# Optimization experiments

Hardware: AMD Instinct MI355X
Metric: run time of the kernel (lower is better)

The kernel has to match this reference:

```python
import jax, jax.numpy as jnp
import numpy as np

B, C, H, W = 8, 48, 192, 192
N = H * W


def _bn_train(x, gamma, beta, eps=1e-5):
    # BatchNorm2d in training mode: biased batch stats over (B, H, W) per channel
    mean = jnp.mean(x, axis=(0, 2, 3), keepdims=True)
    var = jnp.var(x, axis=(0, 2, 3), keepdims=True)
    xn = (x - mean) * jax.lax.rsqrt(var + eps)
    return xn * gamma[None, :, None, None] + beta[None, :, None, None]


def _conv(x, w, b, pad):
    y = jax.lax.conv_general_dilated(
        x, w, window_strides=(1, 1), padding=[(pad, pad), (pad, pad)],
        dimension_numbers=('NCHW', 'OIHW', 'NCHW'))
    return y + b[None, :, None, None]


def setup_inputs() -> dict:
    key = jax.random.key(0)
    ks = jax.random.split(key, 16)
    s = 0.05
    inp = {
        'input_feature': jax.random.normal(ks[0], (B, C, H, W), jnp.float32),
        'fb': jax.random.normal(ks[1], (B, C, H, W), jnp.float32),
        'fc': jax.random.normal(ks[2], (B, C, H, W), jnp.float32),
        'fd': jax.random.normal(ks[3], (B, C, H, W), jnp.float32),
        'Wa': jax.random.normal(ks[4], (C, C), jnp.float32) * s,
        'Wb': jax.random.normal(ks[5], (C, C), jnp.float32) * s,
        'Wc': jax.random.normal(ks[6], (C, C), jnp.float32) * s,
        'Wd': jax.random.normal(ks[7], (C, C), jnp.float32) * s,
        'fuse_w': jax.random.normal(ks[8], (C, 4 * C, 1, 1), jnp.float32) * s,
        'fuse_b': jnp.zeros((C,), jnp.float32),
        'fuse_gamma': jnp.ones((C,), jnp.float32),
        'fuse_beta': jnp.zeros((C,), jnp.float32),
        'gamma_cam': jnp.full((1,), 0.5, jnp.float32),  # nn.Parameter (init 0; nonzero for testing)
        'out_w': jax.random.normal(ks[9], (C, C, 3, 3), jnp.float32) * s,
        'out_b': jnp.zeros((C,), jnp.float32),
        'out_gamma': jnp.ones((C,), jnp.float32),
        'out_beta': jnp.zeros((C,), jnp.float32),
    }
    return inp


def reference(input_feature, fb, fc, fd, Wa, Wb, Wc, Wd,
              fuse_w, fuse_b, fuse_gamma, fuse_beta, gamma_cam,
              out_w, out_b, out_gamma, out_beta):
    b, c, h, w = input_feature.shape
    n = h * w
    # Linear over channel dim: x.view(B,C,N).permute -> [B,N,C] @ W.T -> permute back = [B,C,N]
    def lin(x, Wm):
        return jnp.einsum('oc,bcn->bon', Wm, x.reshape(b, c, n))

    q = lin(input_feature, Wa)                      # [B,C,N] shared query
    K = jnp.stack([q, lin(fb, Wb), lin(fc, Wc), lin(fd, Wd)], axis=0)  # [4,B,C,N] (k==v)

    # Fused 4-branch channel attention: energy [4,B,C,C]
    energy = jnp.einsum('bcn,sbdn->sbcd', q, K)
    energy_new = jnp.max(energy, axis=-1, keepdims=True) - energy  # reversed softmax logits
    attention = jax.nn.softmax(energy_new, axis=-1)
    out4 = jnp.einsum('sbcd,sbdn->sbcn', attention, K)              # [4,B,C,N]

    # concat along channel dim in branch order -> [B,4C,H,W]
    cat = out4.transpose(1, 0, 2, 3).reshape(b, 4 * c, h, w)

    atten = jax.nn.relu(_bn_train(_conv(cat, fuse_w, fuse_b, pad=0), fuse_gamma, fuse_beta))
    out = gamma_cam[0] * atten + input_feature
    out = jax.nn.relu(_bn_train(_conv(out, out_w, out_b, pad=1), out_gamma, out_beta))
    return out
```

## Files before the change

### kernel.cpp

```cpp
#include <hip/hip_runtime.h>
#include <hip/hip_bf16.h>

#define C 48
#define C4 192
#define HW 192
#define NPIX (HW * HW)
#define BATCH 8
#define CNT (BATCH * NPIX)

#define APRE_OFF   0ull
#define G_OFF      14155776ull
#define STATS_OFF  14229504ull
#define M2_OFF     14229696ull
#define MIDT_BYTE  57213696ull
#define WB_BYTE    85525248ull

typedef __attribute__((ext_vector_type(8))) short short8;
typedef __attribute__((ext_vector_type(4))) float f32x4;

static __device__ __forceinline__ unsigned pkbf(float a, float b) {
    union { __hip_bfloat162 h; unsigned u; } t;
    t.h = __float22bfloat162_rn(make_float2(a, b));
    return t.u;
}
static __device__ __forceinline__ float lo2f(unsigned p) { return __uint_as_float(p << 16); }
static __device__ __forceinline__ float hi2f(unsigned p) { return __uint_as_float(p & 0xffff0000u); }
static __device__ __forceinline__ short f2bfs(float f) { return (short)(pkbf(f, f) & 0xffffu); }

__global__ __launch_bounds__(256, 3) void k_gram_mfma(
    const float* __restrict__ x0, const float* __restrict__ x1,
    const float* __restrict__ x2, const float* __restrict__ x3,
    float* __restrict__ G)
{
    __shared__ short hibuf[C4 * 68];
    __shared__ short lobuf[C4 * 68];
    int b = blockIdx.y;
    int n0 = blockIdx.x * 256;
    int tid = threadIdx.x;
    int wid = tid >> 6, lane = tid & 63, col = lane & 15, quad = lane >> 4;

    const float* x0b = x0 + (size_t)b * C * NPIX;
    const float* x1b = x1 + (size_t)b * C * NPIX;
    const float* x2b = x2 + (size_t)b * C * NPIX;
    const float* x3b = x3 + (size_t)b * C * NPIX;

    f32x4 acc[3][3];
#pragma unroll
    for (int mt = 0; mt < 3; ++mt)
#pragma unroll
        for (int nt = 0; nt < 3; ++nt)
            acc[mt][nt] = (f32x4){0.f, 0.f, 0.f, 0.f};

    int scr = tid >> 4;
    int n4 = (tid & 15) * 4;

#define GRAM_LOAD(dst, nb)                                                      \
    _Pragma("unroll")                                                           \
    for (int it = 0; it < 12; ++it) {                                           \
        const float* xb = (it / 3 == 0) ? x0b : (it / 3 == 1) ? x1b             \
                        : (it / 3 == 2) ? x2b : x3b;                            \
        dst[it] = *(const float4*)(xb + (size_t)(scr + (it % 3) * 16) * NPIX    \
                                      + (nb) + n4);                             \
    }

#define GRAM_PACK(src)                                                          \
    _Pragma("unroll")                                                           \
    for (int it = 0; it < 12; ++it) {                                           \
        int ch = scr + it * 16;                                                 \
        float4 v = src[it];                                                     \
        unsigned h01 = pkbf(v.x, v.y), h23 = pkbf(v.z, v.w);                    \
        float r0 = v.x - lo2f(h01), r1 = v.y - hi2f(h01);                       \
        float r2 = v.z - lo2f(h23), r3 = v.w - hi2f(h23);                       \
        unsigned l01 = pkbf(r0, r1), l23 = pkbf(r2, r3);                        \
        *(uint2*)&hibuf[ch * 68 + n4] = make_uint2(h01, h23);                   \
        *(uint2*)&lobuf[ch * 68 + n4] = make_uint2(l01, l23);                   \
    }

#define GRAM_MMA()                                                              \
    _Pragma("unroll")                                                           \
    for (int kb = 0; kb < 2; ++kb) {                                            \
        int ko = kb * 32 + quad * 8;                                            \
        short8 ah[3], al[3], bh[3], bl[3];                                      \
        _Pragma("unroll")                                                       \
        for (int mt = 0; mt < 3; ++mt) {                                        \
            ah[mt] = *(const short8*)&hibuf[(mt * 16 + col) * 68 + ko];         \
            al[mt] = *(const short8*)&lobuf[(mt * 16 + col) * 68 + ko];         \
        }                                                                       \
        _Pragma("unroll")                                                       \
        for (int nt = 0; nt < 3; ++nt) {                                        \
            int row = (wid * 3 + nt) * 16 + col;                                \
            bh[nt] = *(const short8*)&hibuf[row * 68 + ko];                     \
            bl[nt] = *(const short8*)&lobuf[row * 68 + ko];                     \
        }                                                                       \
        _Pragma("unroll")                                                       \
        for (int mt = 0; mt < 3; ++mt)                                          \
            _Pragma("unroll")                                                   \
            for (int nt = 0; nt < 3; ++nt) {                                    \
                acc[mt][nt] = __builtin_amdgcn_mfma_f32_16x16x32_bf16(          \
                    ah[mt], bh[nt], acc[mt][nt], 0, 0, 0);                      \
                acc[mt][nt] = __builtin_amdgcn_mfma_f32_16x16x32_bf16(          \
                    ah[mt], bl[nt], acc[mt][nt], 0, 0, 0);                      \
                acc[mt][nt] = __builtin_amdgcn_mfma_f32_16x16x32_bf16(          \
                    al[mt], bh[nt], acc[mt][nt], 0, 0, 0);                      \
            }                                                                   \
    }

    float4 preA[12], preB[12];
    GRAM_LOAD(preA, n0)
    GRAM_LOAD(preB, n0 + 64)

#pragma unroll
    for (int sp = 0; sp < 2; ++sp) {
        GRAM_PACK(preA)
        __syncthreads();
        if (sp < 1) { GRAM_LOAD(preA, n0 + (2 * sp + 2) * 64) }
        GRAM_MMA()
        __syncthreads();
        GRAM_PACK(preB)
        __syncthreads();
        if (sp < 1) { GRAM_LOAD(preB, n0 + (2 * sp + 3) * 64) }
        GRAM_MMA()
        __syncthreads();
    }
#undef GRAM_LOAD
#undef GRAM_PACK
#undef GRAM_MMA

#pragma unroll
    for (int mt = 0; mt < 3; ++mt)
#pragma unroll
        for (int nt = 0; nt < 3; ++nt) {
            int g = (wid * 3 + nt) * 16 + col;
            int s = g / C, d = g - s * C;
#pragma unroll
            for (int j = 0; j < 4; ++j) {
                int c = mt * 16 + quad * 4 + j;
                atomicAdd(&G[(((size_t)s * BATCH + b) * C + c) * C + d],
                          acc[mt][nt][j]);
            }
        }
}

__global__ __launch_bounds__(256) void k_small(
    const float* __restrict__ G,
    const float* __restrict__ Wa, const float* __restrict__ Wb,
    const float* __restrict__ Wc, const float* __restrict__ Wd,
    const float* __restrict__ fuse_w, float* __restrict__ M2g)
{
    int s = blockIdx.x, b = blockIdx.y;
    const float* Ws = (s == 0) ? Wa : (s == 1) ? Wb : (s == 2) ? Wc : Wd;

    __shared__ float g[C * C], wsm[C * C], wam[C * C], fw[C * C];
    __shared__ float t[C * C], e[C * C], m[C * C];
    int tid = threadIdx.x;

    const float* Gb = G + ((size_t)s * BATCH + b) * C * C;
    for (int k = tid; k < C * C; k += 256) {
        g[k] = Gb[k];
        wsm[k] = Ws[k];
        wam[k] = Wa[k];
        int o = k / C, c = k % C;
        fw[k] = fuse_w[(size_t)o * C4 + s * C + c];
    }
    __syncthreads();

    for (int k = tid; k < C * C; k += 256) {
        int c = k / C, d = k % C;
        float a = 0.f;
        for (int q = 0; q < C; ++q) a += g[c * C + q] * wsm[d * C + q];
        t[k] = a;
    }
    __syncthreads();
    for (int k = tid; k < C * C; k += 256) {
        int c = k / C, d = k % C;
        float a = 0.f;
        for (int q = 0; q < C; ++q) a += wam[c * C + q] * t[q * C + d];
        e[k] = a;
    }
    __syncthreads();
    if (tid < C) {
        int c = tid;
        float mn = e[c * C];
        for (int d = 1; d < C; ++d) mn = fminf(mn, e[c * C + d]);
        float sum = 0.f;
        for (int d = 0; d < C; ++d) {
            float v = __expf(mn - e[c * C + d]);
            e[c * C + d] = v;
            sum += v;
        }
        float inv = 1.0f / sum;
        for (int d = 0; d < C; ++d) e[c * C + d] *= inv;
    }
    __syncthreads();
    for (int k = tid; k < C * C; k += 256) {
        int d = k / C, o = k % C;
        float a = 0.f;
        for (int q = 0; q < C; ++q) a += fw[o * C + q] * e[q * C + d];
        m[k] = a;
    }
    __syncthreads();
    float* out = M2g + ((size_t)b * 4 + s) * C * C;
    for (int k = tid; k < C * C; k += 256) {
        int c = k / C, o = k % C;
        float a = 0.f;
        for (int q = 0; q < C; ++q) a += wsm[q * C + c] * m[q * C + o];
        out[k] = a;
    }
}

static __device__ __forceinline__ unsigned ladr(unsigned row, unsigned x) {
    unsigned f = ((row >> 1) ^ (row >> 2)) & 7;
    return (row << 9) | (x ^ (f << 4));
}

__global__ __launch_bounds__(256) void k_apply_mfma(
    const float* __restrict__ x0, const float* __restrict__ x1,
    const float* __restrict__ x2, const float* __restrict__ x3,
    const float* __restrict__ M2g, const float* __restrict__ fuse_b,
    float* __restrict__ apre, float* __restrict__ stats)
{
    __shared__ __align__(16) char xbuf[64 * 512];
    __shared__ float sst[96];
    char* lb = xbuf;

    int b = blockIdx.y;
    int n0 = blockIdx.x * 256;
    int tid = threadIdx.x;
    int wid = tid >> 6, lane = tid & 63, col = lane & 15, quad = lane >> 4;

    const float* x0b = x0 + (size_t)b * C * NPIX;
    const float* x1b = x1 + (size_t)b * C * NPIX;
    const float* x2b = x2 + (size_t)b * C * NPIX;
    const float* x3b = x3 + (size_t)b * C * NPIX;

    if (tid < 96) sst[tid] = 0.f;

    const float* Mb = M2g + (size_t)b * 4 * C * C;
    for (int e = tid; e < 48 * 192; e += 256) {
        int k = e / 48, o = e - k * 48;
        *(short*)(lb + ladr(o, k * 2)) = f2bfs(Mb[(size_t)k * 48 + o]);
    }
    __syncthreads();

    short8 afr[3][6];
#pragma unroll
    for (int mt = 0; mt < 3; ++mt)
#pragma unroll
        for (int kq = 0; kq < 6; ++kq)
            afr[mt][kq] = *(const short8*)(lb + ladr(mt * 16 + col, kq * 64 + quad * 16));

    float fbv[3][4];
#pragma unroll
    for (int mt = 0; mt < 3; ++mt)
#pragma unroll
        for (int j = 0; j < 4; ++j)
            fbv[mt][j] = fuse_b[mt * 16 + quad * 4 + j];

    float s1[3][4] = {}, s2[3][4] = {};
    int nl = (wid << 4) + col;

    for (int sub = 0; sub < 4; ++sub) {
        int nb = n0 + sub * 64;
        __syncthreads();
#pragma unroll
        for (int it = 0; it < 6; ++it) {
            int ef = tid + it * 256;
            int p  = ef >> 4;
            int nq = (ef & 15) << 2;
            int s  = p / 24;
            int c2 = (p - s * 24) * 2;
            const float* xp = ((s == 0) ? x0b : (s == 1) ? x1b : (s == 2) ? x2b : x3b)
                              + (size_t)c2 * NPIX + nb + nq;
            float4 va = *(const float4*)xp;
            float4 vb = *(const float4*)(xp + NPIX);
            unsigned p4 = (unsigned)p * 4;
            *(unsigned*)(lb + ladr(nq + 0, p4)) = pkbf(va.x, vb.x);
            *(unsigned*)(lb + ladr(nq + 1, p4)) = pkbf(va.y, vb.y);
            *(unsigned*)(lb + ladr(nq + 2, p4)) = pkbf(va.z, vb.z);
            *(unsigned*)(lb + ladr(nq + 3, p4)) = pkbf(va.w, vb.w);
        }
        __syncthreads();

        f32x4 acc[3];
        acc[0] = (f32x4){0.f, 0.f, 0.f, 0.f};
        acc[1] = (f32x4){0.f, 0.f, 0.f, 0.f};
        acc[2] = (f32x4){0.f, 0.f, 0.f, 0.f};
#pragma unroll
        for (int kq = 0; kq < 6; ++kq) {
            short8 bfr = *(const short8*)(lb + ladr(nl, kq * 64 + quad * 16));
            acc[0] = __builtin_amdgcn_mfma_f32_16x16x32_bf16(afr[0][kq], bfr, acc[0], 0, 0, 0);
            acc[1] = __builtin_amdgcn_mfma_f32_16x16x32_bf16(afr[1][kq], bfr, acc[1], 0, 0, 0);
            acc[2] = __builtin_amdgcn_mfma_f32_16x16x32_bf16(afr[2][kq], bfr, acc[2], 0, 0, 0);
        }

        int n = nb + nl;
#pragma unroll
        for (int mt = 0; mt < 3; ++mt)
#pragma unroll
            for (int j = 0; j < 4; ++j) {
                int o = mt * 16 + quad * 4 + j;
                float val = acc[mt][j] + fbv[mt][j];
                apre[((size_t)b * C + o) * NPIX + n] = val;
                s1[mt][j] += val;
                s2[mt][j] += val * val;
            }
    }

#pragma unroll
    for (int mt = 0; mt < 3; ++mt)
#pragma unroll
        for (int j = 0; j < 4; ++j) {
            float a = s1[mt][j], q = s2[mt][j];
#pragma unroll
            for (int off = 8; off; off >>= 1) {
                a += __shfl_down(a, off, 16);
                q += __shfl_down(q, off, 16);
            }
            if (col == 0) {
                int o = mt * 16 + quad * 4 + j;
                atomicAdd(&sst[o], a);
                atomicAdd(&sst[48 + o], q);
            }
        }
    __syncthreads();
    if (tid < 96) atomicAdd(&stats[tid], sst[tid]);
}

__global__ __launch_bounds__(256) void k_bn1t(
    const float* __restrict__ apre, const float* __restrict__ inp,
    const float* __restrict__ stats, const float* __restrict__ gamma,
    const float* __restrict__ beta, const float* __restrict__ gcam,
    short* __restrict__ mid_t)
{
    __shared__ short t[64 * C];
    int b = blockIdx.y;
    int n0 = blockIdx.x * 64;
    int tid = threadIdx.x;
    const float invc = 1.0f / (float)CNT;
    float g = gcam[0];

#pragma unroll
    for (int it = 0; it < 3; ++it) {
        int e = tid + it * 256;
        int c = e >> 4, pq = (e & 15) * 4;
        float mu = stats[c] * invc;
        float var = stats[C + c] * invc - mu * mu;
        float sc = gamma[c] * rsqrtf(var + 1e-5f);
        float be = beta[c] - mu * sc;
        size_t base = ((size_t)b * C + c) * NPIX + n0 + pq;
        float4 v = *(const float4*)(apre + base);
        float4 x = *(const float4*)(inp + base);
        t[(pq + 0) * C + c] = f2bfs(fmaxf(v.x * sc + be, 0.f) * g + x.x);
        t[(pq + 1) * C + c] = f2bfs(fmaxf(v.y * sc + be, 0.f) * g + x.y);
        t[(pq + 2) * C + c] = f2bfs(fmaxf(v.z * sc + be, 0.f) * g + x.z);
        t[(pq + 3) * C + c] = f2bfs(fmaxf(v.w * sc + be, 0.f) * g + x.w);
    }
    __syncthreads();
    short* mb = mid_t + ((size_t)b * NPIX + n0) * C;
#pragma unroll
    for (int it = 0; it < 3; ++it) {
        int e = tid + it * 256;
        *(short4*)(mb + e * 4) = *(const short4*)&t[e * 4];
    }
}

__global__ __launch_bounds__(256) void k_prep(
    const float* __restrict__ outw, short* __restrict__ Wb)
{
    int idx = blockIdx.x * 256 + threadIdx.x;
    if (idx >= 9 * 48 * 64) return;
    int i = idx & 63;
    int o = (idx >> 6) % 48;
    int tap = idx / (64 * 48);
    float v = (i < C) ? outw[((size_t)o * C + i) * 9 + tap] : 0.f;
    Wb[idx] = f2bfs(v);
}

__global__ __launch_bounds__(256) void k_conv_mfma(
    const short* __restrict__ mid_t, const short* __restrict__ Wb,
    const float* __restrict__ bias, float* __restrict__ out,
    float* __restrict__ stats)
{
    __shared__ short xl[324 * 72];
    __shared__ float sst[96];
    int b = blockIdx.y;
    int ty = blockIdx.x / 12, tx = blockIdx.x % 12;
    int h0 = ty * 16, w0 = tx * 16;
    int tid = threadIdx.x;

    if (tid < 96) sst[tid] = 0.f;

    for (int ch = tid; ch < 2916; ch += 256) {
        int lpx = ch / 9, part = ch % 9;
        int hh = h0 - 1 + lpx / 18, ww = w0 - 1 + lpx % 18;
        short8 v = {0, 0, 0, 0, 0, 0, 0, 0};
        if (part < 6 && hh >= 0 && hh < HW && ww >= 0 && ww < HW)
            v = *(const short8*)(mid_t + ((size_t)b * NPIX + hh * HW + ww) * C + part * 8);
        *(short8*)(xl + lpx * 72 + part * 8) = v;
    }
    __syncthreads();

    int wid = tid >> 6, lane = tid & 63;
    int col = lane & 15, quad = lane >> 4;

    f32x4 acc[3][4];
#pragma unroll
    for (int mt = 0; mt < 3; ++mt)
#pragma unroll
        for (int rr = 0; rr < 4; ++rr)
            acc[mt][rr] = (f32x4){0.f, 0.f, 0.f, 0.f};

#pragma unroll
    for (int tap = 0; tap < 9; ++tap) {
        int dh = tap / 3, dw = tap % 3;
#pragma unroll
        for (int kb = 0; kb < 2; ++kb) {
            short8 afr[3];
#pragma unroll
            for (int mt = 0; mt < 3; ++mt)
                afr[mt] = *(const short8*)(Wb + ((size_t)(tap * 48 + mt * 16 + col)) * 64
                                               + kb * 32 + quad * 8);
#pragma unroll
            for (int rr = 0; rr < 4; ++rr) {
                int r = wid * 4 + rr;
                int lpx = (r + dh) * 18 + col + dw;
                short8 bfr = *(const short8*)(xl + lpx * 72 + kb * 32 + quad * 8);
#pragma unroll
                for (int mt = 0; mt < 3; ++mt)
                    acc[mt][rr] = __builtin_amdgcn_mfma_f32_16x16x32_bf16(
                        afr[mt], bfr, acc[mt][rr], 0, 0, 0);
            }
        }
    }

    float s1[3][4] = {}, s2[3][4] = {};
#pragma unroll
    for (int mt = 0; mt < 3; ++mt)
#pragma unroll
        for (int rr = 0; rr < 4; ++rr) {
            int r = wid * 4 + rr;
            f32x4 v = acc[mt][rr];
#pragma unroll
            for (int j = 0; j < 4; ++j) {
                int o = mt * 16 + quad * 4 + j;
                float val = v[j] + bias[o];
                out[((size_t)b * C + o) * NPIX + (h0 + r) * HW + w0 + col] = val;
                s1[mt][j] += val;
                s2[mt][j] += val * val;
            }
        }
#pragma unroll
    for (int mt = 0; mt < 3; ++mt)
#pragma unroll
        for (int j = 0; j < 4; ++j) {
            float a = s1[mt][j], q = s2[mt][j];
#pragma unroll
            for (int off = 8; off; off >>= 1) {
                a += __shfl_down(a, off, 16);
                q += __shfl_down(q, off, 16);
            }
            if (col == 0) {
                int o = mt * 16 + quad * 4 + j;
                atomicAdd(&sst[o], a);
                atomicAdd(&sst[48 + o], q);
            }
        }
    __syncthreads();
    if (tid < 48)       atomicAdd(&stats[2 * C + tid], sst[tid]);
    else if (tid < 96)  atomicAdd(&stats[3 * C + tid - 48], sst[tid]);
}

__global__ __launch_bounds__(256) void k_bn2(
    float* __restrict__ out, const float* __restrict__ stats,
    const float* __restrict__ gamma, const float* __restrict__ beta)
{
    size_t i = ((size_t)blockIdx.x * 256 + threadIdx.x) * 4;
    int c = (int)((i / NPIX) % C);
    const float invc = 1.0f / (float)CNT;
    float mu = stats[2 * C + c] * invc;
    float var = stats[3 * C + c] * invc - mu * mu;
    float sc = gamma[c] * rsqrtf(var + 1e-5f);
    float be = beta[c] - mu * sc;

    float4 v = *(float4*)(out + i);
    v.x = fmaxf(v.x * sc + be, 0.f);
    v.y = fmaxf(v.y * sc + be, 0.f);
    v.z = fmaxf(v.z * sc + be, 0.f);
    v.w = fmaxf(v.w * sc + be, 0.f);
    *(float4*)(out + i) = v;
}

extern "C" void kernel_launch(void* const* d_in, const int* in_sizes, int n_in,
                              void* d_out, int out_size, void* d_ws, size_t ws_size,
                              hipStream_t stream)
{
    const float* inp   = (const float*)d_in[0];
    const float* fb    = (const float*)d_in[1];
    const float* fc    = (const float*)d_in[2];
    const float* fd    = (const float*)d_in[3];
    const float* Wa    = (const float*)d_in[4];
    const float* Wbm   = (const float*)d_in[5];
    const float* Wcm   = (const float*)d_in[6];
    const float* Wdm   = (const float*)d_in[7];
    const float* fusew = (const float*)d_in[8];
    const float* fuseb = (const float*)d_in[9];
    const float* fgam  = (const float*)d_in[10];
    const float* fbet  = (const float*)d_in[11];
    const float* gcam  = (const float*)d_in[12];
    const float* outw  = (const float*)d_in[13];
    const float* outb  = (const float*)d_in[14];
    const float* ogam  = (const float*)d_in[15];
    const float* obet  = (const float*)d_in[16];

    float* ws    = (float*)d_ws;
    float* apre  = ws + APRE_OFF;
    float* G     = ws + G_OFF;
    float* stats = ws + STATS_OFF;
    float* M2g   = ws + M2_OFF;
    short* mid_t = (short*)((char*)d_ws + MIDT_BYTE);
    short* Wb    = (short*)((char*)d_ws + WB_BYTE);
    float* out   = (float*)d_out;

    hipMemsetAsync(G, 0, (73728ull + 192ull) * sizeof(float), stream);

    k_prep<<<108, 256, 0, stream>>>(outw, Wb);
    k_gram_mfma<<<dim3(144, BATCH), 256, 0, stream>>>(inp, fb, fc, fd, G);
    k_small<<<dim3(4, BATCH), 256, 0, stream>>>(G, Wa, Wbm, Wcm, Wdm, fusew, M2g);
    k_apply_mfma<<<dim3(144, BATCH), 256, 0, stream>>>(inp, fb, fc, fd, M2g, fuseb, apre, stats);
    k_bn1t<<<dim3(576, BATCH), 256, 0, stream>>>(apre, inp, stats, fgam, fbet, gcam, mid_t);
    k_conv_mfma<<<dim3(144, BATCH), 256, 0, stream>>>(mid_t, Wb, outb, out, stats);
    k_bn2<<<13824, 256, 0, stream>>>(out, stats, ogam, obet);
}
```

Measured before the change: 511.3 us.

## Stage gram tiles with async global_load_lds and split to bf16 at MMA time

The gram kernel now copies raw fp32 tiles straight from global memory into a double-buffered, XOR-swizzled LDS tile using global_load_lds. This replaces the register prefetch and the hi/lo bf16 packing done before the LDS store. The hi/lo split now happens after the LDS read, just before the MFMAs, and explicit vmcnt waits plus barriers overlap the next tile's load with the current compute. The cost is more repeated packing work per wave (each wave re-packs the A rows), larger LDS use, and occupancy lowered to 2 blocks per SIMD.

Result: faster. 477.3 us (-6.6%).

```diff
diff --git a/kernel.cpp b/kernel.cpp
--- a/kernel.cpp
+++ b/kernel.cpp
@@ -27,13 +27,23 @@
 static __device__ __forceinline__ float hi2f(unsigned p) { return __uint_as_float(p & 0xffff0000u); }
 static __device__ __forceinline__ short f2bfs(float f) { return (short)(pkbf(f, f) & 0xffffu); }
 
-__global__ __launch_bounds__(256, 3) void k_gram_mfma(
+static __device__ __forceinline__ void pk8(f32x4 g0, f32x4 g1, short8& hi, short8& lo) {
+    union { short8 s; unsigned u[4]; } H, L;
+    H.u[0] = pkbf(g0[0], g0[1]); H.u[1] = pkbf(g0[2], g0[3]);
+    H.u[2] = pkbf(g1[0], g1[1]); H.u[3] = pkbf(g1[2], g1[3]);
+    L.u[0] = pkbf(g0[0] - lo2f(H.u[0]), g0[1] - hi2f(H.u[0]));
+    L.u[1] = pkbf(g0[2] - lo2f(H.u[1]), g0[3] - hi2f(H.u[1]));
+    L.u[2] = pkbf(g1[0] - lo2f(H.u[2]), g1[1] - hi2f(H.u[2]));
+    L.u[3] = pkbf(g1[2] - lo2f(H.u[3]), g1[3] - hi2f(H.u[3]));
+    hi = H.s; lo = L.s;
+}
+
+__global__ __launch_bounds__(256, 2) void k_gram_mfma(
     const float* __restrict__ x0, const float* __restrict__ x1,
     const float* __restrict__ x2, const float* __restrict__ x3,
     float* __restrict__ G)
 {
-    __shared__ short hibuf[C4 * 68];
-    __shared__ short lobuf[C4 * 68];
+    __shared__ float tile[2][192 * 32];
     int b = blockIdx.y;
     int n0 = blockIdx.x * 256;
     int tid = threadIdx.x;
@@ -43,6 +53,11 @@
     const float* x1b = x1 + (size_t)b * C * NPIX;
     const float* x2b = x2 + (size_t)b * C * NPIX;
     const float* x3b = x3 + (size_t)b * C * NPIX;
+    const float* xw = (wid == 0) ? x0b : (wid == 1) ? x1b : (wid == 2) ? x2b : x3b;
+
+    int r8 = lane >> 3;
+    int sl = (lane & 7) ^ r8;
+    const float* srcbase = xw + (size_t)r8 * NPIX + sl * 4;
 
     f32x4 acc[3][3];
 #pragma unroll
@@ -51,80 +66,69 @@
         for (int nt = 0; nt < 3; ++nt)
             acc[mt][nt] = (f32x4){0.f, 0.f, 0.f, 0.f};
 
-    int scr = tid >> 4;
-    int n4 = (tid & 15) * 4;
-
-#define GRAM_LOAD(dst, nb)                                                      \
-    _Pragma("unroll")                                                           \
-    for (int it = 0; it < 12; ++it) {                                           \
-        const float* xb = (it / 3 == 0) ? x0b : (it / 3 == 1) ? x1b             \
-                        : (it / 3 == 2) ? x2b : x3b;                            \
-        dst[it] = *(const float4*)(xb + (size_t)(scr + (it % 3) * 16) * NPIX    \
-                                      + (nb) + n4);                             \
-    }
-
-#define GRAM_PACK(src)                                                          \
-    _Pragma("unroll")                                                           \
-    for (int it = 0; it < 12; ++it) {                                           \
-        int ch = scr + it * 16;                                                 \
-        float4 v = src[it];                                                     \
-        unsigned h01 = pkbf(v.x, v.y), h23 = pkbf(v.z, v.w);                    \
-        float r0 = v.x - lo2f(h01), r1 = v.y - hi2f(h01);                       \
-        float r2 = v.z - lo2f(h23), r3 = v.w - hi2f(h23);                       \
-        unsigned l01 = pkbf(r0, r1), l23 = pkbf(r2, r3);                        \
-        *(uint2*)&hibuf[ch * 68 + n4] = make_uint2(h01, h23);                   \
-        *(uint2*)&lobuf[ch * 68 + n4] = make_uint2(l01, l23);                   \
-    }
-
-#define GRAM_MMA()                                                              \
-    _Pragma("unroll")                                                           \
-    for (int kb = 0; kb < 2; ++kb) {                                            \
-        int ko = kb * 32 + quad * 8;                                            \
-        short8 ah[3], al[3], bh[3], bl[3];                                      \
+    int r7 = col & 7;
+    int q2 = quad * 2;
+
+#define STAGE(buf, nb)                                                          \
+    {                                                                           \
+        char* dstb = (char*)&tile[buf][0] + wid * 6144;                         \
+        const float* sb = srcbase + (nb);                                       \
+        _Pragma("unroll")                                                       \
+        for (int j = 0; j < 6; ++j)                                             \
+            __builtin_amdgcn_global_load_lds(                                   \
+                (const __attribute__((address_space(1))) void*)                 \
+                    (sb + (size_t)8 * j * NPIX),                                \
+                (__attribute__((address_space(3))) void*)(dstb + j * 1024),     \
+                16, 0, 0);                                                      \
+    }
+
+#define COMPUTE(buf)                                                            \
+    {                                                                           \
+        const char* tb = (const char*)&tile[buf][0];                            \
+        short8 ah[3], al[3];                                                    \
         _Pragma("unroll")                                                       \
         for (int mt = 0; mt < 3; ++mt) {                                        \
-            ah[mt] = *(const short8*)&hibuf[(mt * 16 + col) * 68 + ko];         \
-            al[mt] = *(const short8*)&lobuf[(mt * 16 + col) * 68 + ko];         \
+            int row = mt * 16 + col;                                            \
+            f32x4 g0 = *(const f32x4*)(tb + row * 128 + ((q2 ^ r7) << 4));      \
+            f32x4 g1 = *(const f32x4*)(tb + row * 128 + (((q2 + 1) ^ r7) << 4));\
+            pk8(g0, g1, ah[mt], al[mt]);                                        \
         }                                                                       \
         _Pragma("unroll")                                                       \
         for (int nt = 0; nt < 3; ++nt) {                                        \
             int row = (wid * 3 + nt) * 16 + col;                                \
-            bh[nt] = *(const short8*)&hibuf[row * 68 + ko];                     \
-            bl[nt] = *(const short8*)&lobuf[row * 68 + ko];                     \
+            f32x4 g0 = *(const f32x4*)(tb + row * 128 + ((q2 ^ r7) << 4));      \
+            f32x4 g1 = *(const f32x4*)(tb + row * 128 + (((q2 + 1) ^ r7) << 4));\
+            short8 bh, bl;                                                      \
+            pk8(g0, g1, bh, bl);                                                \
+            _Pragma("unroll")                                                   \
+            for (int mt = 0; mt < 3; ++mt) {                                    \
+                acc[mt][nt] = __builtin_amdgcn_mfma_f32_16x16x32_bf16(          \
+                    ah[mt], bh, acc[mt][nt], 0, 0, 0);                          \
+                acc[mt][nt] = __builtin_amdgcn_mfma_f32_16x16x32_bf16(          \
+                    ah[mt], bl, acc[mt][nt], 0, 0, 0);                          \
+                acc[mt][nt] = __builtin_amdgcn_mfma_f32_16x16x32_bf16(          \
+                    al[mt], bh, acc[mt][nt], 0, 0, 0);                          \
+            }                                                                   \
         }                                                                       \
-        _Pragma("unroll")                                                       \
-        for (int mt = 0; mt < 3; ++mt)                                          \
-            _Pragma("unroll")                                                   \
-            for (int nt = 0; nt < 3; ++nt) {                                    \
-                acc[mt][nt] = __builtin_amdgcn_mfma_f32_16x16x32_bf16(          \
-                    ah[mt], bh[nt], acc[mt][nt], 0, 0, 0);                      \
-                acc[mt][nt] = __builtin_amdgcn_mfma_f32_16x16x32_bf16(          \
-                    ah[mt], bl[nt], acc[mt][nt], 0, 0, 0);                      \
-                acc[mt][nt] = __builtin_amdgcn_mfma_f32_16x16x32_bf16(          \
-                    al[mt], bh[nt], acc[mt][nt], 0, 0, 0);                      \
-            }                                                                   \
-    }
-
-    float4 preA[12], preB[12];
-    GRAM_LOAD(preA, n0)
-    GRAM_LOAD(preB, n0 + 64)
-
-#pragma unroll
-    for (int sp = 0; sp < 2; ++sp) {
-        GRAM_PACK(preA)
-        __syncthreads();
-        if (sp < 1) { GRAM_LOAD(preA, n0 + (2 * sp + 2) * 64) }
-        GRAM_MMA()
-        __syncthreads();
-        GRAM_PACK(preB)
-        __syncthreads();
-        if (sp < 1) { GRAM_LOAD(preB, n0 + (2 * sp + 3) * 64) }
-        GRAM_MMA()
-        __syncthreads();
-    }
-#undef GRAM_LOAD
-#undef GRAM_PACK
-#undef GRAM_MMA
+    }
+
+    STAGE(0, n0)
+    for (int t = 0; t < 8; ++t) {
+        if (t < 7) {
+            STAGE((t + 1) & 1, n0 + (t + 1) * 32)
+            asm volatile("s_waitcnt vmcnt(6)" ::: "memory");
+        } else {
+            asm volatile("s_waitcnt vmcnt(0)" ::: "memory");
+        }
+        __builtin_amdgcn_sched_barrier(0);
+        __builtin_amdgcn_s_barrier();
+        __builtin_amdgcn_sched_barrier(0);
+        COMPUTE(t & 1)
+        __builtin_amdgcn_s_barrier();
+        __builtin_amdgcn_sched_barrier(0);
+    }
+#undef STAGE
+#undef COMPUTE
 
 #pragma unroll
     for (int mt = 0; mt < 3; ++mt)
```
